# Performance work log

Hardware: AMD Instinct MI355X
Metric: run time of the kernel (lower is better)

## Reference

```python
import jax, jax.numpy as jnp
import numpy as np

EMBED_DIM = 1024
NUM_HEADS = 16
HEAD_DIM = EMBED_DIM // NUM_HEADS  # 64


def setup_inputs() -> dict:
    key = jax.random.key(0)
    k1, k2, k3 = jax.random.split(key, 3)
    B, N = 2, 2048
    x = jax.random.normal(k1, (B, N, EMBED_DIM), dtype=jnp.float32)
    # torch nn.Linear(E, 3E): y = x @ W.T + b; we store W already transposed as [E, 3E]
    W_qkv = jax.random.normal(k2, (EMBED_DIM, 3 * EMBED_DIM), dtype=jnp.float32) * (EMBED_DIM ** -0.5)
    b_qkv = jax.random.normal(k3, (3 * EMBED_DIM,), dtype=jnp.float32) * 0.02
    return {"x": x, "W_qkv": W_qkv, "b_qkv": b_qkv}


def reference(x, W_qkv, b_qkv):
    B, N, E = x.shape
    H, e = NUM_HEADS, HEAD_DIM
    y = x @ W_qkv + b_qkv                      # [B, N, 3E]
    # einops: 'b n (e k) -> b n e k' (k=3) then 'b n (e H) k -> b H n e k'
    # => flat index into 3E is (e_idx*H + h)*3 + qkv_idx
    y = y.reshape(B, N, e, H, 3)
    y = jnp.transpose(y, (0, 3, 1, 2, 4))      # [B, H, N, e, 3]
    q, k, v = y[..., 0], y[..., 1], y[..., 2]  # each [B, H, N, e]
    scale = 1.0 / jnp.sqrt(jnp.asarray(H, dtype=x.dtype))  # note: sqrt(num_heads), per source
    scores = jnp.einsum('bhne,bhme->bhnm', q, k) * scale   # [B, H, N, N]
    wei = jax.nn.softmax(scores, axis=-1)
    out = jnp.einsum('bhnm,bhme->bhne', wei, v)            # [B, H, N, e]
    # 'b H n e -> b n (H e)'; dropout is identity in eval mode
    out = jnp.transpose(out, (0, 2, 1, 3)).reshape(B, N, H * e)
    return out
```

## Files before the change

### kernel.cpp

```cpp
#include <hip/hip_runtime.h>
#include <hip/hip_bf16.h>
#include <math.h>

#define EDIM 1024
#define N3E  3072
#define NSEQ 2048
#define NB   2
#define NH   16
#define HD   64
#define MTOT (NB*NSEQ)

typedef __attribute__((ext_vector_type(8))) short bf16x8;
typedef __attribute__((ext_vector_type(4))) float f32x4;

#define SCALE2 0.360673760222241f
#define DTHR   16.0f

__device__ __forceinline__ short f2bf(float f) {
    union { float f; unsigned u; } v; v.f = f;
    unsigned r = v.u + 0x7FFFu + ((v.u >> 16) & 1u);
    return (short)(r >> 16);
}

__device__ __forceinline__ unsigned cvtpk(float lo, float hi) {
    unsigned r;
    asm("v_cvt_pk_bf16_f32 %0, %1, %2" : "=v"(r) : "v"(lo), "v"(hi));
    return r;
}

__device__ __forceinline__ void gload16(const void* g, void* l) {
    __builtin_amdgcn_global_load_lds(
        (const __attribute__((address_space(1))) unsigned int*)g,
        (__attribute__((address_space(3))) unsigned int*)l, 16, 0, 0);
}

__global__ __launch_bounds__(256) void k_convert_x(const float* __restrict__ x,
                                                   short* __restrict__ xb, int n4) {
    int i = blockIdx.x * blockDim.x + threadIdx.x;
    int stride = gridDim.x * blockDim.x;
    for (; i < n4; i += stride) {
        float4 v = ((const float4*)x)[i];
        ushort4 o;
        o.x = (unsigned short)f2bf(v.x);
        o.y = (unsigned short)f2bf(v.y);
        o.z = (unsigned short)f2bf(v.z);
        o.w = (unsigned short)f2bf(v.w);
        ((ushort4*)xb)[i] = o;
    }
}

__global__ __launch_bounds__(256) void k_transpose_w(const float* __restrict__ w,
                                                     short* __restrict__ wt) {
    __shared__ float T[96][68];
    int k0 = blockIdx.x * 64;
    int c0 = blockIdx.y * 96;
    int t = threadIdx.x;
    {
        int kr = t >> 2;
        int cb = (t & 3) * 24;
        const float* src = w + (size_t)(k0 + kr) * N3E + c0 + cb;
        #pragma unroll
        for (int i = 0; i < 24; i += 4) {
            float4 v = *(const float4*)(src + i);
            T[cb + i + 0][kr] = v.x;
            T[cb + i + 1][kr] = v.y;
            T[cb + i + 2][kr] = v.z;
            T[cb + i + 3][kr] = v.w;
        }
    }
    __syncthreads();
    int kk = (t & 7) * 8;
    #pragma unroll
    for (int p = 0; p < 3; ++p) {
        int cc = p * 32 + (t >> 3);
        int ca = c0 + cc;
        int e = ca / 48, h = (ca % 48) / 3, q = ca % 3;
        int cp = q * 1024 + h * 64 + e;
        bf16x8 o;
        #pragma unroll
        for (int j = 0; j < 8; ++j) o[j] = f2bf(T[cc][kk + j]);
        *(bf16x8*)(wt + (size_t)cp * EDIM + k0 + kk) = o;
    }
}

__global__ void k_perm_bias(const float* __restrict__ b, float* __restrict__ bp) {
    int c = blockIdx.x * 256 + threadIdx.x;
    if (c >= N3E) return;
    int e = c / 48, h = (c % 48) / 3, q = c % 3;
    bp[q * 1024 + h * 64 + e] = b[c];
}

__global__ __launch_bounds__(256) void k_qkv_gemm(const short* __restrict__ xb,
        const short* __restrict__ wt, const float* __restrict__ bp,
        short* __restrict__ qkv) {
    __shared__ short Al[2][128][32];
    __shared__ short Bl[2][128][32];
    int t = threadIdx.x, lane = t & 63, wv = t >> 6;
    int g = lane >> 4, r = lane & 15;
    int wr = wv >> 1, wc = wv & 1;
    int flat = blockIdx.y * 32 + blockIdx.x;
    int sw = (flat & 7) * 96 + (flat >> 3);
    int m0 = (sw & 31) * 128, n0 = (sw >> 5) * 128;
    int srow = wv * 32 + (lane >> 2);
    int scol = (lane & 3) * 8;
    const short* ga0 = xb + (size_t)(m0 + srow) * EDIM + scol;
    const short* ga1 = ga0 + (size_t)16 * EDIM;
    const short* gb0 = wt + (size_t)(n0 + srow) * EDIM + scol;
    const short* gb1 = gb0 + (size_t)16 * EDIM;
    char* laA = (char*)(&Al[0][0][0]) + wv * 2048;
    char* laB = (char*)(&Bl[0][0][0]) + wv * 2048;
    f32x4 acc[4][4] = {};
    gload16(ga0, laA);
    gload16(ga1, laA + 1024);
    gload16(gb0, laB);
    gload16(gb1, laB + 1024);
    __syncthreads();
    for (int step = 0; step < 32; ++step) {
        if (step < 31) {
            int nk = (step + 1) * 32;
            int bo = ((step + 1) & 1) * 8192;
            gload16(ga0 + nk, laA + bo);
            gload16(ga1 + nk, laA + bo + 1024);
            gload16(gb0 + nk, laB + bo);
            gload16(gb1 + nk, laB + bo + 1024);
        }
        int cb = step & 1;
        bf16x8 af[4], bfr[4];
        #pragma unroll
        for (int mt = 0; mt < 4; ++mt)
            af[mt] = *(const bf16x8*)(&Al[cb][wr*64 + mt*16 + r][g*8]);
        #pragma unroll
        for (int nt = 0; nt < 4; ++nt)
            bfr[nt] = *(const bf16x8*)(&Bl[cb][wc*64 + nt*16 + r][g*8]);
        #pragma unroll
        for (int mt = 0; mt < 4; ++mt)
            #pragma unroll
            for (int nt = 0; nt < 4; ++nt)
                acc[mt][nt] = __builtin_amdgcn_mfma_f32_16x16x32_bf16(
                                  af[mt], bfr[nt], acc[mt][nt], 0, 0, 0);
        __syncthreads();
    }
    #pragma unroll
    for (int nt = 0; nt < 4; ++nt) {
        int cp = n0 + wc*64 + nt*16 + r;
        float bias = bp[cp];
        int q = cp >> 10, h = (cp >> 6) & 15, e = cp & 63;
        #pragma unroll
        for (int mt = 0; mt < 4; ++mt) {
            #pragma unroll
            for (int rg = 0; rg < 4; ++rg) {
                int m = m0 + wr*64 + mt*16 + g*4 + rg;
                int bb = m >> 11, n = m & 2047;
                qkv[((((size_t)q*NB + bb)*NH + h)*NSEQ + n)*HD + e] =
                    f2bf(acc[mt][nt][rg] + bias);
            }
        }
    }
}

__global__ __launch_bounds__(256) void k_attn(const short* __restrict__ qkv,
                                              float* __restrict__ out) {
    __shared__ short Kl[64][68];
    __shared__ short Vt[64][68];
    __shared__ short Pl[4][16][64];
    int t = threadIdx.x, lane = t & 63, wv = t >> 6;
    int g = lane >> 4, r = lane & 15;
    int qb = blockIdx.x, h = blockIdx.y, b = blockIdx.z;
    const size_t HS = (size_t)NSEQ * HD;
    const short* Qp = qkv + ((size_t)(0*NB + b)*NH + h) * HS;
    const short* Kp = qkv + ((size_t)(1*NB + b)*NH + h) * HS;
    const short* Vp = qkv + ((size_t)(2*NB + b)*NH + h) * HS;
    int q0 = qb * 64 + wv * 16;
    bf16x8 qf0 = *(const bf16x8*)(Qp + (size_t)(q0 + r)*HD + g*8);
    bf16x8 qf1 = *(const bf16x8*)(Qp + (size_t)(q0 + r)*HD + 32 + g*8);
    f32x4 o[4] = {};
    float mr = -3.0e38f, lr = 0.f;
    int skv = t >> 2, sd = (t & 3) * 16;
    int vkv = (t >> 4) * 4, vd = (t & 15) * 4;
    int rx = (r & 7) << 4;
    char* prow = (char*)(&Pl[wv][0][0]) + r * 128;
    bf16x8 kk0, kk1; ushort4 vv0, vv1, vv2, vv3;
    const short* Kst = Kp + (size_t)skv * HD + sd;
    const short* Vst = Vp + (size_t)vkv * HD + vd;
    kk0 = *(const bf16x8*)(Kst);
    kk1 = *(const bf16x8*)(Kst + 8);
    vv0 = *(const ushort4*)(Vst);
    vv1 = *(const ushort4*)(Vst + HD);
    vv2 = *(const ushort4*)(Vst + 2*HD);
    vv3 = *(const ushort4*)(Vst + 3*HD);
    {
        *(bf16x8*)(&Kl[skv][sd]) = kk0;
        *(bf16x8*)(&Kl[skv][sd + 8]) = kk1;
        #pragma unroll
        for (int i = 0; i < 4; ++i) {
            unsigned lo = (unsigned)((const unsigned short*)&vv0)[i]
                        | ((unsigned)((const unsigned short*)&vv1)[i] << 16);
            unsigned hi = (unsigned)((const unsigned short*)&vv2)[i]
                        | ((unsigned)((const unsigned short*)&vv3)[i] << 16);
            uint2 wrd; wrd.x = lo; wrd.y = hi;
            *(uint2*)(&Vt[vd + i][vkv]) = wrd;
        }
    }
    for (int kt = 0; kt < NSEQ; kt += 64) {
        __syncthreads();
        bool more = (kt + 64) < NSEQ;
        if (more) {
            kk0 = *(const bf16x8*)(Kst + (size_t)(kt + 64) * HD);
            kk1 = *(const bf16x8*)(Kst + (size_t)(kt + 64) * HD + 8);
            vv0 = *(const ushort4*)(Vst + (size_t)(kt + 64) * HD);
            vv1 = *(const ushort4*)(Vst + (size_t)(kt + 65) * HD);
            vv2 = *(const ushort4*)(Vst + (size_t)(kt + 66) * HD);
            vv3 = *(const ushort4*)(Vst + (size_t)(kt + 67) * HD);
        }
        f32x4 s[4];
        #pragma unroll
        for (int jt = 0; jt < 4; ++jt) {
            bf16x8 kf0 = *(const bf16x8*)(&Kl[jt*16 + r][g*8]);
            bf16x8 kf1 = *(const bf16x8*)(&Kl[jt*16 + r][32 + g*8]);
            f32x4 z = {};
            s[jt] = __builtin_amdgcn_mfma_f32_16x16x32_bf16(kf0, qf0, z, 0,0,0);
            s[jt] = __builtin_amdgcn_mfma_f32_16x16x32_bf16(kf1, qf1, s[jt], 0,0,0);
        }
        bf16x8 vf[4][2];
        #pragma unroll
        for (int dt = 0; dt < 4; ++dt) {
            vf[dt][0] = *(const bf16x8*)(&Vt[dt*16 + r][g*8]);
            vf[dt][1] = *(const bf16x8*)(&Vt[dt*16 + r][32 + g*8]);
        }
        float mx = fmaxf(fmaxf(fmaxf(s[0][0], s[0][1]), fmaxf(s[0][2], s[0][3])),
                         fmaxf(fmaxf(s[1][0], s[1][1]), fmaxf(s[1][2], s[1][3])));
        mx = fmaxf(mx, fmaxf(fmaxf(fmaxf(s[2][0], s[2][1]), fmaxf(s[2][2], s[2][3])),
                             fmaxf(fmaxf(s[3][0], s[3][1]), fmaxf(s[3][2], s[3][3]))));
        mx = fmaxf(mx, __shfl_xor(mx, 16));
        mx = fmaxf(mx, __shfl_xor(mx, 32));
        if (!__all(mx <= mr + DTHR)) {
            float mnew = fmaxf(mr, mx);
            float a = exp2f(SCALE2 * (mr - mnew));
            mr = mnew;
            lr *= a;
            #pragma unroll
            for (int dt = 0; dt < 4; ++dt) o[dt] *= a;
        }
        float cm = SCALE2 * mr;
        float ps = 0.f;
        #pragma unroll
        for (int jt = 0; jt < 4; ++jt) {
            float p0 = exp2f(fmaf(SCALE2, s[jt][0], -cm));
            float p1 = exp2f(fmaf(SCALE2, s[jt][1], -cm));
            float p2 = exp2f(fmaf(SCALE2, s[jt][2], -cm));
            float p3 = exp2f(fmaf(SCALE2, s[jt][3], -cm));
            ps += (p0 + p1) + (p2 + p3);
            uint2 wrd; wrd.x = cvtpk(p0, p1); wrd.y = cvtpk(p2, p3);
            *(uint2*)(prow + ((32*jt + 8*g) ^ rx)) = wrd;
        }
        ps += __shfl_xor(ps, 16);
        ps += __shfl_xor(ps, 32);
        lr += ps;
        bf16x8 pb0 = *(const bf16x8*)(prow + ((16*g) ^ rx));
        bf16x8 pb1 = *(const bf16x8*)(prow + ((64 + 16*g) ^ rx));
        #pragma unroll
        for (int dt = 0; dt < 4; ++dt) {
            o[dt] = __builtin_amdgcn_mfma_f32_16x16x32_bf16(vf[dt][0], pb0, o[dt], 0,0,0);
            o[dt] = __builtin_amdgcn_mfma_f32_16x16x32_bf16(vf[dt][1], pb1, o[dt], 0,0,0);
        }
        __syncthreads();
        if (more) {
            *(bf16x8*)(&Kl[skv][sd]) = kk0;
            *(bf16x8*)(&Kl[skv][sd + 8]) = kk1;
            #pragma unroll
            for (int i = 0; i < 4; ++i) {
                unsigned lo = (unsigned)((const unsigned short*)&vv0)[i]
                            | ((unsigned)((const unsigned short*)&vv1)[i] << 16);
                unsigned hi = (unsigned)((const unsigned short*)&vv2)[i]
                            | ((unsigned)((const unsigned short*)&vv3)[i] << 16);
                uint2 wrd; wrd.x = lo; wrd.y = hi;
                *(uint2*)(&Vt[vd + i][vkv]) = wrd;
            }
        }
    }
    float inv = 1.0f / lr;
    #pragma unroll
    for (int dt = 0; dt < 4; ++dt) {
        float4 v0;
        v0.x = o[dt][0]*inv; v0.y = o[dt][1]*inv;
        v0.z = o[dt][2]*inv; v0.w = o[dt][3]*inv;
        *(float4*)(out + (size_t)(b*NSEQ + q0 + r)*EDIM + h*HD + dt*16 + g*4) = v0;
    }
}

extern "C" void kernel_launch(void* const* d_in, const int* in_sizes, int n_in,
                              void* d_out, int out_size, void* d_ws, size_t ws_size,
                              hipStream_t stream) {
    const float* x  = (const float*)d_in[0];
    const float* w  = (const float*)d_in[1];
    const float* bq = (const float*)d_in[2];
    float* outp = (float*)d_out;
    char* ws = (char*)d_ws;
    short* Xb  = (short*)(ws);
    short* Wt  = (short*)(ws + 8388608);
    float* Bp  = (float*)(ws + 8388608 + 6291456);
    short* QKV = (short*)(ws + 8388608 + 6291456 + 16384);
    k_convert_x<<<dim3(2048), dim3(256), 0, stream>>>(x, Xb, (MTOT*EDIM)/4);
    k_transpose_w<<<dim3(16, 32), dim3(256), 0, stream>>>(w, Wt);
    k_perm_bias<<<dim3(12), dim3(256), 0, stream>>>(bq, Bp);
    k_qkv_gemm<<<dim3(32, 24), dim3(256), 0, stream>>>(Xb, Wt, Bp, QKV);
    k_attn<<<dim3(32, 16, 2), dim3(256), 0, stream>>>(QKV, outp);
}
```

Measured before the change: 220.6 us.

## Switch attention to 32x32x16 MFMA with register-resident P via permlane swap

Rewrites the attention inner loop so each wave handles 32 query rows using 32x32x16 bf16 MFMAs instead of 16x16x32. The softmax probabilities stay in registers and are rearranged into the B-operand layout with v_permlane32_swap, which removes the per-wave LDS round trip for P. Each block now covers 128 queries, so the grid is halved and every K/V tile staged in LDS is reused by twice as many queries. The cost is higher register pressure from the 16-wide accumulators and fewer blocks to fill the GPU.

```diff
diff --git a/kernel.cpp b/kernel.cpp
--- a/kernel.cpp
+++ b/kernel.cpp
@@ -12,6 +12,7 @@
 
 typedef __attribute__((ext_vector_type(8))) short bf16x8;
 typedef __attribute__((ext_vector_type(4))) float f32x4;
+typedef __attribute__((ext_vector_type(16))) float f32x16;
 
 #define SCALE2 0.360673760222241f
 #define DTHR   16.0f
@@ -26,6 +27,10 @@
     unsigned r;
     asm("v_cvt_pk_bf16_f32 %0, %1, %2" : "=v"(r) : "v"(lo), "v"(hi));
     return r;
+}
+
+__device__ __forceinline__ void pl32swap(unsigned &a, unsigned &b) {
+    asm volatile("v_permlane32_swap_b32 %0, %1" : "+v"(a), "+v"(b));
 }
 
 __device__ __forceinline__ void gload16(const void* g, void* l) {
@@ -162,23 +167,22 @@
                                               float* __restrict__ out) {
     __shared__ short Kl[64][68];
     __shared__ short Vt[64][68];
-    __shared__ short Pl[4][16][64];
     int t = threadIdx.x, lane = t & 63, wv = t >> 6;
-    int g = lane >> 4, r = lane & 15;
-    int qb = blockIdx.x, h = blockIdx.y, b = blockIdx.z;
+    int cq = lane & 31, hf = lane >> 5;
+    int qb = blockIdx.x, hd = blockIdx.y, b = blockIdx.z;
     const size_t HS = (size_t)NSEQ * HD;
-    const short* Qp = qkv + ((size_t)(0*NB + b)*NH + h) * HS;
-    const short* Kp = qkv + ((size_t)(1*NB + b)*NH + h) * HS;
-    const short* Vp = qkv + ((size_t)(2*NB + b)*NH + h) * HS;
-    int q0 = qb * 64 + wv * 16;
-    bf16x8 qf0 = *(const bf16x8*)(Qp + (size_t)(q0 + r)*HD + g*8);
-    bf16x8 qf1 = *(const bf16x8*)(Qp + (size_t)(q0 + r)*HD + 32 + g*8);
-    f32x4 o[4] = {};
+    const short* Qp = qkv + ((size_t)(0*NB + b)*NH + hd) * HS;
+    const short* Kp = qkv + ((size_t)(1*NB + b)*NH + hd) * HS;
+    const short* Vp = qkv + ((size_t)(2*NB + b)*NH + hd) * HS;
+    int q0 = qb * 128 + wv * 32;
+    bf16x8 qf[4];
+    #pragma unroll
+    for (int ks = 0; ks < 4; ++ks)
+        qf[ks] = *(const bf16x8*)(Qp + (size_t)(q0 + cq)*HD + 16*ks + 8*hf);
+    f32x16 o0 = {}, o1 = {};
     float mr = -3.0e38f, lr = 0.f;
     int skv = t >> 2, sd = (t & 3) * 16;
     int vkv = (t >> 4) * 4, vd = (t & 15) * 4;
-    int rx = (r & 7) << 4;
-    char* prow = (char*)(&Pl[wv][0][0]) + r * 128;
     bf16x8 kk0, kk1; ushort4 vv0, vv1, vv2, vv3;
     const short* Kst = Kp + (size_t)skv * HD + sd;
     const short* Vst = Vp + (size_t)vkv * HD + vd;
@@ -212,56 +216,60 @@
             vv2 = *(const ushort4*)(Vst + (size_t)(kt + 66) * HD);
             vv3 = *(const ushort4*)(Vst + (size_t)(kt + 67) * HD);
         }
-        f32x4 s[4];
-        #pragma unroll
-        for (int jt = 0; jt < 4; ++jt) {
-            bf16x8 kf0 = *(const bf16x8*)(&Kl[jt*16 + r][g*8]);
-            bf16x8 kf1 = *(const bf16x8*)(&Kl[jt*16 + r][32 + g*8]);
-            f32x4 z = {};
-            s[jt] = __builtin_amdgcn_mfma_f32_16x16x32_bf16(kf0, qf0, z, 0,0,0);
-            s[jt] = __builtin_amdgcn_mfma_f32_16x16x32_bf16(kf1, qf1, s[jt], 0,0,0);
-        }
-        bf16x8 vf[4][2];
-        #pragma unroll
-        for (int dt = 0; dt < 4; ++dt) {
-            vf[dt][0] = *(const bf16x8*)(&Vt[dt*16 + r][g*8]);
-            vf[dt][1] = *(const bf16x8*)(&Vt[dt*16 + r][32 + g*8]);
-        }
-        float mx = fmaxf(fmaxf(fmaxf(s[0][0], s[0][1]), fmaxf(s[0][2], s[0][3])),
-                         fmaxf(fmaxf(s[1][0], s[1][1]), fmaxf(s[1][2], s[1][3])));
-        mx = fmaxf(mx, fmaxf(fmaxf(fmaxf(s[2][0], s[2][1]), fmaxf(s[2][2], s[2][3])),
-                             fmaxf(fmaxf(s[3][0], s[3][1]), fmaxf(s[3][2], s[3][3]))));
-        mx = fmaxf(mx, __shfl_xor(mx, 16));
+        f32x16 s0 = {}, s1 = {};
+        #pragma unroll
+        for (int ks = 0; ks < 4; ++ks) {
+            bf16x8 kf0 = *(const bf16x8*)(&Kl[cq][16*ks + 8*hf]);
+            bf16x8 kf1 = *(const bf16x8*)(&Kl[32 + cq][16*ks + 8*hf]);
+            s0 = __builtin_amdgcn_mfma_f32_32x32x16_bf16(kf0, qf[ks], s0, 0, 0, 0);
+            s1 = __builtin_amdgcn_mfma_f32_32x32x16_bf16(kf1, qf[ks], s1, 0, 0, 0);
+        }
+        bf16x8 vf0[4], vf1[4];
+        #pragma unroll
+        for (int m = 0; m < 4; ++m) {
+            vf0[m] = *(const bf16x8*)(&Vt[cq][16*m + 8*hf]);
+            vf1[m] = *(const bf16x8*)(&Vt[32 + cq][16*m + 8*hf]);
+        }
+        float mx = s0[0];
+        #pragma unroll
+        for (int e = 1; e < 16; ++e) mx = fmaxf(mx, s0[e]);
+        #pragma unroll
+        for (int e = 0; e < 16; ++e) mx = fmaxf(mx, s1[e]);
         mx = fmaxf(mx, __shfl_xor(mx, 32));
         if (!__all(mx <= mr + DTHR)) {
             float mnew = fmaxf(mr, mx);
             float a = exp2f(SCALE2 * (mr - mnew));
-            mr = mnew;
-            lr *= a;
+            mr = mnew; lr *= a;
             #pragma unroll
-            for (int dt = 0; dt < 4; ++dt) o[dt] *= a;
+            for (int e = 0; e < 16; ++e) { o0[e] *= a; o1[e] *= a; }
         }
         float cm = SCALE2 * mr;
         float ps = 0.f;
-        #pragma unroll
-        for (int jt = 0; jt < 4; ++jt) {
-            float p0 = exp2f(fmaf(SCALE2, s[jt][0], -cm));
-            float p1 = exp2f(fmaf(SCALE2, s[jt][1], -cm));
-            float p2 = exp2f(fmaf(SCALE2, s[jt][2], -cm));
-            float p3 = exp2f(fmaf(SCALE2, s[jt][3], -cm));
-            ps += (p0 + p1) + (p2 + p3);
-            uint2 wrd; wrd.x = cvtpk(p0, p1); wrd.y = cvtpk(p2, p3);
-            *(uint2*)(prow + ((32*jt + 8*g) ^ rx)) = wrd;
-        }
-        ps += __shfl_xor(ps, 16);
+        unsigned pa[8], pb[8];
+        #pragma unroll
+        for (int i = 0; i < 8; ++i) {
+            float x0 = exp2f(fmaf(SCALE2, s0[2*i],   -cm));
+            float x1 = exp2f(fmaf(SCALE2, s0[2*i+1], -cm));
+            float y0 = exp2f(fmaf(SCALE2, s1[2*i],   -cm));
+            float y1 = exp2f(fmaf(SCALE2, s1[2*i+1], -cm));
+            ps += (x0 + x1) + (y0 + y1);
+            pa[i] = cvtpk(x0, x1);
+            pb[i] = cvtpk(y0, y1);
+        }
         ps += __shfl_xor(ps, 32);
         lr += ps;
-        bf16x8 pb0 = *(const bf16x8*)(prow + ((16*g) ^ rx));
-        bf16x8 pb1 = *(const bf16x8*)(prow + ((64 + 16*g) ^ rx));
-        #pragma unroll
-        for (int dt = 0; dt < 4; ++dt) {
-            o[dt] = __builtin_amdgcn_mfma_f32_16x16x32_bf16(vf[dt][0], pb0, o[dt], 0,0,0);
-            o[dt] = __builtin_amdgcn_mfma_f32_16x16x32_bf16(vf[dt][1], pb1, o[dt], 0,0,0);
+        #pragma unroll
+        for (int m = 0; m < 4; ++m) {
+            int mp = m & 1;
+            unsigned w0, w1, w2, w3;
+            if (m < 2) { w0 = pa[4*mp]; w1 = pa[4*mp+1]; w2 = pa[4*mp+2]; w3 = pa[4*mp+3]; }
+            else       { w0 = pb[4*mp]; w1 = pb[4*mp+1]; w2 = pb[4*mp+2]; w3 = pb[4*mp+3]; }
+            pl32swap(w0, w2);
+            pl32swap(w1, w3);
+            union { unsigned u[4]; bf16x8 v; } pu;
+            pu.u[0] = w0; pu.u[1] = w1; pu.u[2] = w2; pu.u[3] = w3;
+            o0 = __builtin_amdgcn_mfma_f32_32x32x16_bf16(vf0[m], pu.v, o0, 0, 0, 0);
+            o1 = __builtin_amdgcn_mfma_f32_32x32x16_bf16(vf1[m], pu.v, o1, 0, 0, 0);
         }
         __syncthreads();
         if (more) {
@@ -279,12 +287,16 @@
         }
     }
     float inv = 1.0f / lr;
+    float* dst = out + (size_t)(b*NSEQ + q0 + cq)*EDIM + hd*HD;
     #pragma unroll
-    for (int dt = 0; dt < 4; ++dt) {
-        float4 v0;
-        v0.x = o[dt][0]*inv; v0.y = o[dt][1]*inv;
-        v0.z = o[dt][2]*inv; v0.w = o[dt][3]*inv;
-        *(float4*)(out + (size_t)(b*NSEQ + q0 + r)*EDIM + h*HD + dt*16 + g*4) = v0;
+    for (int rq = 0; rq < 4; ++rq) {
+        float4 v0, v1;
+        v0.x = o0[4*rq+0]*inv; v0.y = o0[4*rq+1]*inv;
+        v0.z = o0[4*rq+2]*inv; v0.w = o0[4*rq+3]*inv;
+        v1.x = o1[4*rq+0]*inv; v1.y = o1[4*rq+1]*inv;
+        v1.z = o1[4*rq+2]*inv; v1.w = o1[4*rq+3]*inv;
+        *(float4*)(dst + 8*rq + 4*hf)      = v0;
+        *(float4*)(dst + 8*rq + 4*hf + 32) = v1;
     }
 }
 
@@ -304,5 +316,5 @@
     k_transpose_w<<<dim3(16, 32), dim3(256), 0, stream>>>(w, Wt);
     k_perm_bias<<<dim3(12), dim3(256), 0, stream>>>(bq, Bp);
     k_qkv_gemm<<<dim3(32, 24), dim3(256), 0, stream>>>(Xb, Wt, Bp, QKV);
-    k_attn<<<dim3(32, 16, 2), dim3(256), 0, stream>>>(QKV, outp);
-}
+    k_attn<<<dim3(16, 16, 2), dim3(256), 0, stream>>>(QKV, outp);
+}
```

Result: faster. 194.3 us (-11.9%).
